# Kernel optimization log

Hardware: AMD Instinct MI355X
Metric: run time of the kernel (lower is better)

Reference implementation:

```python
import jax, jax.numpy as jnp
import numpy as np

B, S, H = 2, 2048, 1024
NH, DH = 16, 64  # num_attention_heads, attention_head_size


def setup_inputs() -> dict:
    key = jax.random.key(0)
    ks = jax.random.split(key, 5)
    scale = 1.0 / np.sqrt(H)
    return {
        "hidden_states": jax.random.normal(ks[0], (B, S, H), dtype=jnp.float32),
        "bias": jax.random.normal(ks[1], (1, NH, S, S), dtype=jnp.float32),
        "Wq": jax.random.normal(ks[2], (H, H), dtype=jnp.float32) * scale,
        "bq": jnp.zeros((H,), dtype=jnp.float32),
        "Wk": jax.random.normal(ks[3], (H, H), dtype=jnp.float32) * scale,
        "bk": jnp.zeros((H,), dtype=jnp.float32),
        "Wv": jax.random.normal(ks[4], (H, H), dtype=jnp.float32) * scale,
        "bv": jnp.zeros((H,), dtype=jnp.float32),
    }


def _heads(x):
    # [B,S,H] -> [B,NH,S,DH]
    return x.reshape(B, S, NH, DH).transpose(0, 2, 1, 3)


def reference(hidden_states, bias, Wq, bq, Wk, bk, Wv, bv):
    q = _heads(hidden_states @ Wq.T + bq)
    k = _heads(hidden_states @ Wk.T + bk)
    v = _heads(hidden_states @ Wv.T + bv)
    scores = jnp.einsum("bhqd,bhkd->bhqk", q, k) / np.sqrt(DH)
    scores = scores + bias  # ALiBi bias, broadcast over batch
    probs = jax.nn.softmax(scores, axis=-1)
    ctx = jnp.einsum("bhqk,bhkd->bhqd", probs, v)
    return ctx.transpose(0, 2, 1, 3).reshape(B, S, H)
```

## Files before the change

### kernel.cpp

```cpp
#include <hip/hip_runtime.h>
#include <hip/hip_bf16.h>
#include <stdint.h>

#define B_  2
#define S_  2048
#define H_  1024
#define NH_ 16
#define DH_ 64

typedef __attribute__((ext_vector_type(8))) short   s16x8;
typedef __attribute__((ext_vector_type(8))) __bf16  bf16x8;
typedef __attribute__((ext_vector_type(4))) float   f32x4;

__device__ __forceinline__ unsigned short f2bf(float f) {
  union { float f; uint32_t u; } v; v.f = f;
  uint32_t u = v.u;
  uint32_t r = (u + 0x7FFFu + ((u >> 16) & 1u)) >> 16;
  return (unsigned short)r;
}

__device__ __forceinline__ void gll16(const void* g, void* l) {
  __builtin_amdgcn_global_load_lds(
      (__attribute__((address_space(1))) void*)(g),
      (__attribute__((address_space(3))) void*)(l), 16, 0, 0);
}

__device__ __forceinline__ f32x4 mfma_bf16(s16x8 a, s16x8 b, f32x4 c) {
  return __builtin_amdgcn_mfma_f32_16x16x32_bf16(
      __builtin_bit_cast(bf16x8, a), __builtin_bit_cast(bf16x8, b), c, 0, 0, 0);
}

__global__ __launch_bounds__(256) void cvt_kernel(const float* __restrict__ src,
                                                  unsigned short* __restrict__ dst,
                                                  int n4) {
  int i = blockIdx.x * blockDim.x + threadIdx.x;
  int stride = gridDim.x * blockDim.x;
  for (; i < n4; i += stride) {
    float4 f = reinterpret_cast<const float4*>(src)[i];
    ushort4 o;
    o.x = f2bf(f.x); o.y = f2bf(f.y); o.z = f2bf(f.z); o.w = f2bf(f.w);
    reinterpret_cast<ushort4*>(dst)[i] = o;
  }
}

__global__ __launch_bounds__(256) void qkv_gemm(
    const unsigned short* __restrict__ hsb,
    const unsigned short* __restrict__ Wb,
    const float* __restrict__ bq, const float* __restrict__ bk,
    const float* __restrict__ bv,
    unsigned short* __restrict__ Qb, unsigned short* __restrict__ Kb,
    unsigned short* __restrict__ Vtb)
{
  __shared__ alignas(16) unsigned short lA[128 * 64];
  __shared__ alignas(16) unsigned short lB[128 * 64];

  const int tid  = threadIdx.x;
  const int lane = tid & 63;
  const int wid  = tid >> 6;
  const int wrow = wid >> 1, wcol = wid & 1;
  const int z  = blockIdx.z;
  const int m0 = blockIdx.x * 128;
  const int n0 = blockIdx.y * 128;
  const int lr = lane & 15;
  const int lq = lane >> 4;

  const unsigned short* Wz = Wb + (size_t)z * (H_ * H_);

  f32x4 acc[4][4];
  #pragma unroll
  for (int i = 0; i < 4; ++i)
    #pragma unroll
    for (int j = 0; j < 4; ++j) acc[i][j] = {0.f, 0.f, 0.f, 0.f};

  for (int kt = 0; kt < H_ / 64; ++kt) {
    const int k0 = kt * 64;
    __syncthreads();
    #pragma unroll
    for (int i = 0; i < 4; ++i) {
      int idx = i * 256 + tid;
      int row = idx >> 3, cs = idx & 7, c = cs ^ (row & 7);
      gll16(hsb + (size_t)(m0 + row) * H_ + k0 + c * 8, (char*)lA + idx * 16);
    }
    #pragma unroll
    for (int i = 0; i < 4; ++i) {
      int idx = i * 256 + tid;
      int row = idx >> 3, cs = idx & 7, c = cs ^ (row & 7);
      gll16(Wz + (size_t)(n0 + row) * H_ + k0 + c * 8, (char*)lB + idx * 16);
    }
    __syncthreads();

    #pragma unroll
    for (int kk = 0; kk < 2; ++kk) {
      s16x8 af[4], bfr[4];
      #pragma unroll
      for (int mi = 0; mi < 4; ++mi) {
        int row = wrow * 64 + mi * 16 + lr;
        int ch  = (kk * 4 + lq) ^ (row & 7);
        af[mi] = *reinterpret_cast<const s16x8*>((const char*)lA + row * 128 + ch * 16);
      }
      #pragma unroll
      for (int ni = 0; ni < 4; ++ni) {
        int row = wcol * 64 + ni * 16 + lr;
        int ch  = (kk * 4 + lq) ^ (row & 7);
        bfr[ni] = *reinterpret_cast<const s16x8*>((const char*)lB + row * 128 + ch * 16);
      }
      #pragma unroll
      for (int mi = 0; mi < 4; ++mi)
        #pragma unroll
        for (int ni = 0; ni < 4; ++ni)
          acc[mi][ni] = mfma_bf16(af[mi], bfr[ni], acc[mi][ni]);
    }
  }

  const float* bvec = (z == 0) ? bq : (z == 1) ? bk : bv;

  #pragma unroll
  for (int ni = 0; ni < 4; ++ni) {
    int n = n0 + wcol * 64 + ni * 16 + lr;
    float bn = bvec[n];
    int h = n >> 6, d = n & 63;
    #pragma unroll
    for (int mi = 0; mi < 4; ++mi) {
      int mbase = m0 + wrow * 64 + mi * 16 + lq * 4;
      int b = mbase >> 11, s = mbase & 2047;
      if (z == 2) {
        ushort4 o;
        o.x = f2bf(acc[mi][ni][0] + bn);
        o.y = f2bf(acc[mi][ni][1] + bn);
        o.z = f2bf(acc[mi][ni][2] + bn);
        o.w = f2bf(acc[mi][ni][3] + bn);
        *reinterpret_cast<ushort4*>(Vtb + ((size_t)(b * NH_ + h) * DH_ + d) * S_ + s) = o;
      } else {
        unsigned short* dst = (z == 0) ? Qb : Kb;
        #pragma unroll
        for (int j = 0; j < 4; ++j)
          dst[((size_t)(b * NH_ + h) * S_ + (s + j)) * DH_ + d] =
              f2bf(acc[mi][ni][j] + bn);
      }
    }
  }
}

__global__ __launch_bounds__(256) void attn_kernel(
    const unsigned short* __restrict__ Qb,
    const unsigned short* __restrict__ Kb,
    const unsigned short* __restrict__ Vtb,
    const float* __restrict__ bias,
    float* __restrict__ out)
{
  __shared__ alignas(16) unsigned short lK[64 * 64];
  __shared__ alignas(16) unsigned short lV[64 * 64];
  __shared__ alignas(16) unsigned short lP[4][16 * 72];

  const int tid  = threadIdx.x;
  const int lane = tid & 63;
  const int wid  = tid >> 6;
  const int lr = lane & 15, lq = lane >> 4;

  const int q0 = blockIdx.x * 64;
  const int h  = blockIdx.y;
  const int b  = blockIdx.z;
  const int bh = b * NH_ + h;
  const int qrow = q0 + wid * 16 + lr;

  s16x8 qf[2];
  #pragma unroll
  for (int kt = 0; kt < 2; ++kt)
    qf[kt] = *reinterpret_cast<const s16x8*>(
        Qb + ((size_t)bh * S_ + qrow) * DH_ + kt * 32 + lq * 8);

  float m_run = -INFINITY, l_run = 0.0f;
  f32x4 acc_o[4];
  #pragma unroll
  for (int i = 0; i < 4; ++i) acc_o[i] = {0.f, 0.f, 0.f, 0.f};

  const float* brow = bias + ((size_t)h * S_ + qrow) * S_;
  unsigned short* Pw = &lP[wid][0];

  for (int kb = 0; kb < S_ / 64; ++kb) {
    __syncthreads();
    #pragma unroll
    for (int i = 0; i < 2; ++i) {
      int idx = i * 256 + tid;
      int row = idx >> 3, cs = idx & 7, c = cs ^ (row & 7);
      gll16(Kb + ((size_t)bh * S_ + kb * 64 + row) * DH_ + c * 8, (char*)lK + idx * 16);
    }
    #pragma unroll
    for (int i = 0; i < 2; ++i) {
      int idx = i * 256 + tid;
      int row = idx >> 3, cs = idx & 7, c = cs ^ (row & 7);
      gll16(Vtb + ((size_t)bh * DH_ + row) * S_ + kb * 64 + c * 8, (char*)lV + idx * 16);
    }

    float4 b4[4];
    #pragma unroll
    for (int ct = 0; ct < 4; ++ct)
      b4[ct] = *reinterpret_cast<const float4*>(brow + kb * 64 + ct * 16 + lq * 4);

    __syncthreads();

    f32x4 accs[4];
    #pragma unroll
    for (int ct = 0; ct < 4; ++ct) accs[ct] = {0.f, 0.f, 0.f, 0.f};
    #pragma unroll
    for (int ct = 0; ct < 4; ++ct) {
      #pragma unroll
      for (int kt = 0; kt < 2; ++kt) {
        int row = ct * 16 + lr;
        int ch  = (kt * 4 + lq) ^ (row & 7);
        s16x8 kf = *reinterpret_cast<const s16x8*>((const char*)lK + row * 128 + ch * 16);
        accs[ct] = mfma_bf16(kf, qf[kt], accs[ct]);
      }
    }

    float p[16];
    #pragma unroll
    for (int ct = 0; ct < 4; ++ct) {
      p[ct * 4 + 0] = accs[ct][0] * 0.125f + b4[ct].x;
      p[ct * 4 + 1] = accs[ct][1] * 0.125f + b4[ct].y;
      p[ct * 4 + 2] = accs[ct][2] * 0.125f + b4[ct].z;
      p[ct * 4 + 3] = accs[ct][3] * 0.125f + b4[ct].w;
    }
    float tmax = -INFINITY;
    #pragma unroll
    for (int i = 0; i < 16; ++i) tmax = fmaxf(tmax, p[i]);
    tmax = fmaxf(tmax, __shfl_xor(tmax, 16));
    tmax = fmaxf(tmax, __shfl_xor(tmax, 32));

    float m_new = fmaxf(m_run, tmax);
    float alpha = __expf(m_run - m_new);
    float lsum = 0.0f;
    #pragma unroll
    for (int i = 0; i < 16; ++i) { p[i] = __expf(p[i] - m_new); lsum += p[i]; }
    lsum += __shfl_xor(lsum, 16);
    lsum += __shfl_xor(lsum, 32);
    l_run = l_run * alpha + lsum;
    m_run = m_new;

    #pragma unroll
    for (int i = 0; i < 4; ++i) {
      acc_o[i][0] *= alpha; acc_o[i][1] *= alpha;
      acc_o[i][2] *= alpha; acc_o[i][3] *= alpha;
    }

    #pragma unroll
    for (int ct = 0; ct < 4; ++ct) {
      ushort4 o;
      o.x = f2bf(p[ct * 4 + 0]); o.y = f2bf(p[ct * 4 + 1]);
      o.z = f2bf(p[ct * 4 + 2]); o.w = f2bf(p[ct * 4 + 3]);
      *reinterpret_cast<ushort4*>(Pw + lr * 72 + ct * 16 + lq * 4) = o;
    }

    #pragma unroll
    for (int kt = 0; kt < 2; ++kt) {
      s16x8 pf = *reinterpret_cast<const s16x8*>(Pw + lr * 72 + kt * 32 + lq * 8);
      #pragma unroll
      for (int df = 0; df < 4; ++df) {
        int row = df * 16 + lr;
        int ch  = (kt * 4 + lq) ^ (row & 7);
        s16x8 vf = *reinterpret_cast<const s16x8*>((const char*)lV + row * 128 + ch * 16);
        acc_o[df] = mfma_bf16(vf, pf, acc_o[df]);
      }
    }
  }

  float rl = 1.0f / l_run;
  float* orow = out + ((size_t)b * S_ + qrow) * H_ + h * DH_;
  #pragma unroll
  for (int df = 0; df < 4; ++df) {
    float4 o;
    o.x = acc_o[df][0] * rl; o.y = acc_o[df][1] * rl;
    o.z = acc_o[df][2] * rl; o.w = acc_o[df][3] * rl;
    *reinterpret_cast<float4*>(orow + df * 16 + lq * 4) = o;
  }
}

extern "C" void kernel_launch(void* const* d_in, const int* in_sizes, int n_in,
                              void* d_out, int out_size, void* d_ws, size_t ws_size,
                              hipStream_t stream) {
  const float* hs   = (const float*)d_in[0];
  const float* bias = (const float*)d_in[1];
  const float* Wq   = (const float*)d_in[2];
  const float* bq   = (const float*)d_in[3];
  const float* Wk   = (const float*)d_in[4];
  const float* bk   = (const float*)d_in[5];
  const float* Wv   = (const float*)d_in[6];
  const float* bv   = (const float*)d_in[7];
  float* out = (float*)d_out;

  unsigned short* ws  = (unsigned short*)d_ws;
  unsigned short* hsb = ws;
  unsigned short* Wb  = hsb + (size_t)B_ * S_ * H_;
  unsigned short* Qb  = Wb + (size_t)3 * H_ * H_;
  unsigned short* Kb  = Qb + (size_t)B_ * S_ * H_;
  unsigned short* Vtb = Kb + (size_t)B_ * S_ * H_;
  (void)in_sizes; (void)n_in; (void)out_size; (void)ws_size;

  cvt_kernel<<<2048, 256, 0, stream>>>(hs, hsb, (B_ * S_ * H_) / 4);
  cvt_kernel<<<1024, 256, 0, stream>>>(Wq, Wb, (H_ * H_) / 4);
  cvt_kernel<<<1024, 256, 0, stream>>>(Wk, Wb + H_ * H_, (H_ * H_) / 4);
  cvt_kernel<<<1024, 256, 0, stream>>>(Wv, Wb + 2 * H_ * H_, (H_ * H_) / 4);

  dim3 g1(32, 8, 3);
  qkv_gemm<<<g1, 256, 0, stream>>>(hsb, Wb, bq, bk, bv, Qb, Kb, Vtb);

  dim3 g2(32, NH_, B_);
  attn_kernel<<<g2, 256, 0, stream>>>(Qb, Kb, Vtb, bias, out);
}
```

Measured before the change: 504.1 us.

## Double-buffer attention K/V, skip lazy rescale, fold scale into Wq, swizzle grids

The attention loop now double-buffers K/V tiles in LDS and prefetches the next bias tile while computing the current one, which cuts one barrier per iteration. Online-softmax rescaling is skipped unless the running max grows by more than 8 across the wave. The 1/sqrt(DH) scale is folded into the bf16 conversion of Wq and bq. Both GEMM and attention grids are flattened with an XCD-style block swizzle. The bf16 conversion uses the intrinsic instead of manual rounding. Costs are doubled LDS use and more register pressure.

```diff
diff --git a/kernel.cpp b/kernel.cpp
--- a/kernel.cpp
+++ b/kernel.cpp
@@ -13,10 +13,7 @@
 typedef __attribute__((ext_vector_type(4))) float   f32x4;
 
 __device__ __forceinline__ unsigned short f2bf(float f) {
-  union { float f; uint32_t u; } v; v.f = f;
-  uint32_t u = v.u;
-  uint32_t r = (u + 0x7FFFu + ((u >> 16) & 1u)) >> 16;
-  return (unsigned short)r;
+  return __builtin_bit_cast(unsigned short, __float2bfloat16(f));
 }
 
 __device__ __forceinline__ void gll16(const void* g, void* l) {
@@ -32,13 +29,14 @@
 
 __global__ __launch_bounds__(256) void cvt_kernel(const float* __restrict__ src,
                                                   unsigned short* __restrict__ dst,
-                                                  int n4) {
+                                                  int n4, float scale) {
   int i = blockIdx.x * blockDim.x + threadIdx.x;
   int stride = gridDim.x * blockDim.x;
   for (; i < n4; i += stride) {
     float4 f = reinterpret_cast<const float4*>(src)[i];
     ushort4 o;
-    o.x = f2bf(f.x); o.y = f2bf(f.y); o.z = f2bf(f.z); o.w = f2bf(f.w);
+    o.x = f2bf(f.x * scale); o.y = f2bf(f.y * scale);
+    o.z = f2bf(f.z * scale); o.w = f2bf(f.w * scale);
     reinterpret_cast<ushort4*>(dst)[i] = o;
   }
 }
@@ -58,9 +56,11 @@
   const int lane = tid & 63;
   const int wid  = tid >> 6;
   const int wrow = wid >> 1, wcol = wid & 1;
-  const int z  = blockIdx.z;
-  const int m0 = blockIdx.x * 128;
-  const int n0 = blockIdx.y * 128;
+  const int flat = blockIdx.x;
+  const int swz  = (flat & 7) * 96 + (flat >> 3);
+  const int m0 = (swz & 31) * 128;
+  const int n0 = ((swz >> 5) & 7) * 128;
+  const int z  = swz >> 8;
   const int lr = lane & 15;
   const int lq = lane >> 4;
 
@@ -113,11 +113,12 @@
   }
 
   const float* bvec = (z == 0) ? bq : (z == 1) ? bk : bv;
+  const float bscale = (z == 0) ? 0.125f : 1.0f;
 
   #pragma unroll
   for (int ni = 0; ni < 4; ++ni) {
     int n = n0 + wcol * 64 + ni * 16 + lr;
-    float bn = bvec[n];
+    float bn = bvec[n] * bscale;
     int h = n >> 6, d = n & 63;
     #pragma unroll
     for (int mi = 0; mi < 4; ++mi) {
@@ -148,8 +149,8 @@
     const float* __restrict__ bias,
     float* __restrict__ out)
 {
-  __shared__ alignas(16) unsigned short lK[64 * 64];
-  __shared__ alignas(16) unsigned short lV[64 * 64];
+  __shared__ alignas(16) unsigned short lK[2][64 * 64];
+  __shared__ alignas(16) unsigned short lV[2][64 * 64];
   __shared__ alignas(16) unsigned short lP[4][16 * 72];
 
   const int tid  = threadIdx.x;
@@ -157,9 +158,11 @@
   const int wid  = tid >> 6;
   const int lr = lane & 15, lq = lane >> 4;
 
-  const int q0 = blockIdx.x * 64;
-  const int h  = blockIdx.y;
-  const int b  = blockIdx.z;
+  const int flat = blockIdx.x;
+  const int swz  = (flat & 7) * 128 + (flat >> 3);
+  const int q0 = (swz & 31) * 64;
+  const int h  = (swz >> 5) & 15;
+  const int b  = swz >> 9;
   const int bh = b * NH_ + h;
   const int qrow = q0 + wid * 16 + lr;
 
@@ -177,27 +180,36 @@
   const float* brow = bias + ((size_t)h * S_ + qrow) * S_;
   unsigned short* Pw = &lP[wid][0];
 
-  for (int kb = 0; kb < S_ / 64; ++kb) {
-    __syncthreads();
+  auto stage = [&](int buf, int kb) {
     #pragma unroll
     for (int i = 0; i < 2; ++i) {
       int idx = i * 256 + tid;
       int row = idx >> 3, cs = idx & 7, c = cs ^ (row & 7);
-      gll16(Kb + ((size_t)bh * S_ + kb * 64 + row) * DH_ + c * 8, (char*)lK + idx * 16);
-    }
-    #pragma unroll
-    for (int i = 0; i < 2; ++i) {
-      int idx = i * 256 + tid;
-      int row = idx >> 3, cs = idx & 7, c = cs ^ (row & 7);
-      gll16(Vtb + ((size_t)bh * DH_ + row) * S_ + kb * 64 + c * 8, (char*)lV + idx * 16);
-    }
-
-    float4 b4[4];
-    #pragma unroll
-    for (int ct = 0; ct < 4; ++ct)
-      b4[ct] = *reinterpret_cast<const float4*>(brow + kb * 64 + ct * 16 + lq * 4);
-
-    __syncthreads();
+      gll16(Kb + ((size_t)bh * S_ + kb * 64 + row) * DH_ + c * 8,
+            (char*)lK[buf] + idx * 16);
+      gll16(Vtb + ((size_t)bh * DH_ + row) * S_ + kb * 64 + c * 8,
+            (char*)lV[buf] + idx * 16);
+    }
+  };
+
+  stage(0, 0);
+  float4 b4c[4];
+  #pragma unroll
+  for (int ct = 0; ct < 4; ++ct)
+    b4c[ct] = *reinterpret_cast<const float4*>(brow + ct * 16 + lq * 4);
+  __syncthreads();
+
+  for (int kb = 0; kb < S_ / 64; ++kb) {
+    const int cur = kb & 1;
+
+    if (kb + 1 < S_ / 64) stage(cur ^ 1, kb + 1);
+    float4 b4n[4];
+    {
+      int kbn = (kb + 1 < S_ / 64) ? kb + 1 : kb;
+      #pragma unroll
+      for (int ct = 0; ct < 4; ++ct)
+        b4n[ct] = *reinterpret_cast<const float4*>(brow + kbn * 64 + ct * 16 + lq * 4);
+    }
 
     f32x4 accs[4];
     #pragma unroll
@@ -208,7 +220,7 @@
       for (int kt = 0; kt < 2; ++kt) {
         int row = ct * 16 + lr;
         int ch  = (kt * 4 + lq) ^ (row & 7);
-        s16x8 kf = *reinterpret_cast<const s16x8*>((const char*)lK + row * 128 + ch * 16);
+        s16x8 kf = *reinterpret_cast<const s16x8*>((const char*)lK[cur] + row * 128 + ch * 16);
         accs[ct] = mfma_bf16(kf, qf[kt], accs[ct]);
       }
     }
@@ -216,10 +228,10 @@
     float p[16];
     #pragma unroll
     for (int ct = 0; ct < 4; ++ct) {
-      p[ct * 4 + 0] = accs[ct][0] * 0.125f + b4[ct].x;
-      p[ct * 4 + 1] = accs[ct][1] * 0.125f + b4[ct].y;
-      p[ct * 4 + 2] = accs[ct][2] * 0.125f + b4[ct].z;
-      p[ct * 4 + 3] = accs[ct][3] * 0.125f + b4[ct].w;
+      p[ct * 4 + 0] = accs[ct][0] + b4c[ct].x;
+      p[ct * 4 + 1] = accs[ct][1] + b4c[ct].y;
+      p[ct * 4 + 2] = accs[ct][2] + b4c[ct].z;
+      p[ct * 4 + 3] = accs[ct][3] + b4c[ct].w;
     }
     float tmax = -INFINITY;
     #pragma unroll
@@ -227,21 +239,24 @@
     tmax = fmaxf(tmax, __shfl_xor(tmax, 16));
     tmax = fmaxf(tmax, __shfl_xor(tmax, 32));
 
-    float m_new = fmaxf(m_run, tmax);
-    float alpha = __expf(m_run - m_new);
+    if (!__all(tmax - m_run <= 8.0f)) {
+      float m_new = fmaxf(m_run, tmax);
+      float alpha = __expf(m_run - m_new);
+      l_run *= alpha;
+      #pragma unroll
+      for (int i = 0; i < 4; ++i) {
+        acc_o[i][0] *= alpha; acc_o[i][1] *= alpha;
+        acc_o[i][2] *= alpha; acc_o[i][3] *= alpha;
+      }
+      m_run = m_new;
+    }
+
     float lsum = 0.0f;
     #pragma unroll
-    for (int i = 0; i < 16; ++i) { p[i] = __expf(p[i] - m_new); lsum += p[i]; }
+    for (int i = 0; i < 16; ++i) { p[i] = __expf(p[i] - m_run); lsum += p[i]; }
     lsum += __shfl_xor(lsum, 16);
     lsum += __shfl_xor(lsum, 32);
-    l_run = l_run * alpha + lsum;
-    m_run = m_new;
-
-    #pragma unroll
-    for (int i = 0; i < 4; ++i) {
-      acc_o[i][0] *= alpha; acc_o[i][1] *= alpha;
-      acc_o[i][2] *= alpha; acc_o[i][3] *= alpha;
-    }
+    l_run += lsum;
 
     #pragma unroll
     for (int ct = 0; ct < 4; ++ct) {
@@ -258,10 +273,15 @@
       for (int df = 0; df < 4; ++df) {
         int row = df * 16 + lr;
         int ch  = (kt * 4 + lq) ^ (row & 7);
-        s16x8 vf = *reinterpret_cast<const s16x8*>((const char*)lV + row * 128 + ch * 16);
+        s16x8 vf = *reinterpret_cast<const s16x8*>((const char*)lV[cur] + row * 128 + ch * 16);
         acc_o[df] = mfma_bf16(vf, pf, acc_o[df]);
       }
     }
+
+    #pragma unroll
+    for (int ct = 0; ct < 4; ++ct) b4c[ct] = b4n[ct];
+
+    __syncthreads();
   }
 
   float rl = 1.0f / l_run;
@@ -296,14 +316,12 @@
   unsigned short* Vtb = Kb + (size_t)B_ * S_ * H_;
   (void)in_sizes; (void)n_in; (void)out_size; (void)ws_size;
 
-  cvt_kernel<<<2048, 256, 0, stream>>>(hs, hsb, (B_ * S_ * H_) / 4);
-  cvt_kernel<<<1024, 256, 0, stream>>>(Wq, Wb, (H_ * H_) / 4);
-  cvt_kernel<<<1024, 256, 0, stream>>>(Wk, Wb + H_ * H_, (H_ * H_) / 4);
-  cvt_kernel<<<1024, 256, 0, stream>>>(Wv, Wb + 2 * H_ * H_, (H_ * H_) / 4);
-
-  dim3 g1(32, 8, 3);
-  qkv_gemm<<<g1, 256, 0, stream>>>(hsb, Wb, bq, bk, bv, Qb, Kb, Vtb);
-
-  dim3 g2(32, NH_, B_);
-  attn_kernel<<<g2, 256, 0, stream>>>(Qb, Kb, Vtb, bias, out);
-}
+  cvt_kernel<<<2048, 256, 0, stream>>>(hs, hsb, (B_ * S_ * H_) / 4, 1.0f);
+  cvt_kernel<<<1024, 256, 0, stream>>>(Wq, Wb, (H_ * H_) / 4, 0.125f);
+  cvt_kernel<<<1024, 256, 0, stream>>>(Wk, Wb + H_ * H_, (H_ * H_) / 4, 1.0f);
+  cvt_kernel<<<1024, 256, 0, stream>>>(Wv, Wb + 2 * H_ * H_, (H_ * H_) / 4, 1.0f);
+
+  qkv_gemm<<<768, 256, 0, stream>>>(hsb, Wb, bq, bk, bv, Qb, Kb, Vtb);
+
+  attn_kernel<<<1024, 256, 0, stream>>>(Qb, Kb, Vtb, bias, out);
+}
```

Measured after the change: 530.9 us. 1.05x slower.
